# Performance work log

Measured on AMD Instinct MI355X. Metric: run time of the kernel, lower is better.

## Reference

```python
import jax, jax.numpy as jnp
import numpy as np

B, T, D, E = 4, 1024, 1024, 8
HD = 4 * D  # hdim = 4*dim


def setup_inputs() -> dict:
    key = jax.random.key(0)
    k1, k2, k3, k4 = jax.random.split(key, 4)
    std = 0.5 * D ** (-0.5)
    bound = (3.0 ** 0.5) * std
    x = jax.random.normal(k1, (B, T, D), dtype=jnp.float32)
    # router zero-init in source; use small random weights so routing is non-degenerate
    router_w = jax.random.normal(k2, (E, D), dtype=jnp.float32) * 0.02
    expert_fc = jax.random.uniform(k3, (E, D, HD), dtype=jnp.float32, minval=-bound, maxval=bound)
    # proj zero-init in source; use small random so output/backward are non-trivial
    expert_proj = jax.random.normal(k4, (E, D, HD), dtype=jnp.float32) * 0.02
    return {"x": x, "router_w": router_w, "expert_fc": expert_fc, "expert_proj": expert_proj}


def reference(x, router_w, expert_fc, expert_proj):
    # router: Linear(dim, E, bias=False) -> logits [B,T,E]
    logits = jnp.einsum('btd,ed->bte', x, router_w)
    probs = jax.nn.softmax(logits, axis=-1)
    expert_ids = jnp.argmax(probs, axis=-1)  # [B,T]; top-1 (max) routing
    # NOTE: source computes expert_weights (max prob) but does NOT use it in combine.
    mask = jax.nn.one_hot(expert_ids, E, dtype=x.dtype)  # [B,T,E]
    # Dense all-experts compute (faithful to source): h = x @ fc (F.linear with fc.T)
    h = jnp.einsum('btd,edh->ebth', x, expert_fc)
    h = jnp.square(jax.nn.relu(h))  # relu(h)**2
    # expert_output = h @ proj.T (F.linear with proj [dim, hdim])
    out_e = jnp.einsum('ebth,edh->ebtd', h, expert_proj)
    # masked combine: sum_e out_e * (ids == e)
    output = jnp.einsum('ebtd,bte->btd', out_e, mask)
    return output
```

## Files before the change

kernel.cpp:

```cpp
#include <hip/hip_runtime.h>
#include <hip/hip_bf16.h>
#include <stdint.h>

#define NE 8
#define DIM 1024
#define HDIM 4096
#define NTOK 4096
#define KSPLIT 4
#define MAXT 24
#define NT 16

typedef unsigned short ushort_t;
typedef __attribute__((ext_vector_type(4))) float f32x4;
typedef __attribute__((ext_vector_type(8))) short bf16x8;
typedef __attribute__((ext_vector_type(8))) ushort_t u16x8;

#define WAITV(n) asm volatile("s_waitcnt vmcnt(" #n ")" ::: "memory")
#define WAITL0() asm volatile("s_waitcnt lgkmcnt(0)" ::: "memory")
#define WAITL8() asm volatile("s_waitcnt lgkmcnt(8)" ::: "memory")
#define SCHEDB() __builtin_amdgcn_sched_barrier(0)
#define BARRIER() __builtin_amdgcn_s_barrier()

__device__ __forceinline__ ushort_t f2b(float f) {
  union { float f; unsigned u; } c; c.f = f;
  unsigned u = c.u;
  return (ushort_t)((u + 0x7fffu + ((u >> 16) & 1u)) >> 16);
}

__device__ __forceinline__ void gl2lds16(const void* g, void* l) {
  __builtin_amdgcn_global_load_lds(
      (__attribute__((address_space(1))) void*)g,
      (__attribute__((address_space(3))) void*)l, 16, 0, 0);
}

#define PH_MFMA(mh, nh)                                                     \
  { __builtin_amdgcn_s_setprio(1);                                          \
    _Pragma("unroll")                                                       \
    for (int i2 = 0; i2 < 4; ++i2) {                                        \
      _Pragma("unroll")                                                     \
      for (int j2 = 0; j2 < 2; ++j2) {                                      \
        _Pragma("unroll")                                                   \
        for (int kk = 0; kk < 2; ++kk)                                      \
          acc[(mh)*4 + i2][(nh)*2 + j2] =                                   \
            __builtin_amdgcn_mfma_f32_16x16x32_bf16(                        \
              af[i2][kk], bf[(nh)*2 + j2][kk],                              \
              acc[(mh)*4 + i2][(nh)*2 + j2], 0, 0, 0);                      \
      }                                                                     \
    }                                                                       \
    __builtin_amdgcn_s_setprio(0); }

#define LOAD_AF(mh)                                                         \
  { _Pragma("unroll")                                                       \
    for (int i2 = 0; i2 < 4; ++i2) {                                        \
      _Pragma("unroll")                                                     \
      for (int kk = 0; kk < 2; ++kk)                                        \
        af[i2][kk] = *(const bf16x8*)&pA[aBase + ((mh)*64 + i2*16)*64 + ck[kk]]; \
    } }
#define LOAD_BF(nh)                                                         \
  { _Pragma("unroll")                                                       \
    for (int j2 = 0; j2 < 2; ++j2) {                                        \
      _Pragma("unroll")                                                     \
      for (int kk = 0; kk < 2; ++kk)                                        \
        bf[(nh)*2 + j2][kk] = *(const bf16x8*)&pB[bBase + (((nh)*2 + j2)*16)*64 + ck[kk]]; \
    } }

__global__ __launch_bounds__(256) void router_kernel(
    const float* __restrict__ x, const float* __restrict__ rw,
    int* __restrict__ eid, int* __restrict__ rank, int* __restrict__ cnt) {
  __shared__ float w[NE * 1028];
  for (int i = threadIdx.x; i < NE * DIM; i += 256) {
    int e = i >> 10, d = i & 1023;
    w[e * 1028 + d] = rw[i];
  }
  __syncthreads();
  int grp = threadIdx.x >> 3;
  int e = threadIdx.x & 7;
  int t = blockIdx.x * 32 + grp;
  const float4* xr = (const float4*)(x + (size_t)t * DIM);
  const float4* wr = (const float4*)(w + e * 1028);
  float acc = 0.f;
#pragma unroll 4
  for (int i = 0; i < DIM / 4; ++i) {
    float4 xv = xr[i], wv = wr[i];
    acc += xv.x * wv.x + xv.y * wv.y + xv.z * wv.z + xv.w * wv.w;
  }
  float v = acc; int ie = e;
#pragma unroll
  for (int m = 4; m; m >>= 1) {
    float ov = __shfl_xor(v, m, 8);
    int oi = __shfl_xor(ie, m, 8);
    if (ov > v || (ov == v && oi < ie)) { v = ov; ie = oi; }
  }
  if (e == 0) {
    eid[t] = ie;
    rank[t] = atomicAdd(&cnt[ie], 1);
  }
}

__global__ void scan_kernel(const int* __restrict__ cnt, int* __restrict__ offs,
                            int* __restrict__ tile_e, int* __restrict__ tile_m,
                            int* __restrict__ ntiles) {
  if (threadIdx.x == 0) {
    int s = 0, nt = 0;
    for (int e = 0; e < NE; ++e) {
      offs[e] = s;
      int c = cnt[e];
      for (int m = 0; m < c; m += 256) { tile_e[nt] = e; tile_m[nt] = m; ++nt; }
      s += c;
    }
    offs[NE] = s;
    *ntiles = nt;
  }
}

__global__ __launch_bounds__(256) void gather_kernel(
    const float* __restrict__ x, const int* __restrict__ eid,
    const int* __restrict__ rank, const int* __restrict__ offs,
    int* __restrict__ sorted, ushort_t* __restrict__ Xg) {
  int t = blockIdx.x;
  int e = eid[t];
  int pos = offs[e] + rank[t];
  if (threadIdx.x == 0) sorted[pos] = t;
  int i = threadIdx.x;
  float4 v = ((const float4*)(x + (size_t)t * DIM))[i];
  ushort4 o = make_ushort4(f2b(v.x), f2b(v.y), f2b(v.z), f2b(v.w));
  *(ushort4*)(Xg + (size_t)pos * DIM + i * 4) = o;
}

__global__ __launch_bounds__(256) void transpose_fc_kernel(
    const float* __restrict__ fc, ushort_t* __restrict__ fct) {
  __shared__ float tile[64][68];
  int e = blockIdx.z;
  int h0 = blockIdx.x * 64, d0 = blockIdx.y * 64;
  int tid = threadIdx.x;
  int rr = tid >> 4;
  int cc = (tid & 15) * 4;
  const float* src = fc + ((size_t)e * DIM + d0 + rr) * HDIM + h0 + cc;
#pragma unroll
  for (int i = 0; i < 4; ++i) {
    float4 v = *(const float4*)(src + (size_t)(i * 16) * HDIM);
    *(float4*)&tile[rr + i * 16][cc] = v;
  }
  __syncthreads();
  int hr = tid >> 2;
  int dseg = (tid & 3) * 16;
  union { ushort_t s[16]; u16x8 v[2]; } o;
#pragma unroll
  for (int j = 0; j < 16; ++j) o.s[j] = f2b(tile[dseg + j][hr]);
  ushort_t* dst = fct + ((size_t)e * HDIM + h0 + hr) * DIM + d0 + dseg;
  *(u16x8*)dst = o.v[0];
  *(u16x8*)(dst + 8) = o.v[1];
}

#define GEMM_MAIN_LOOP()                                                    \
  stB(0, 0, 0); stB(0, 0, 1); stA(0, 0, 0); stA(0, 0, 1);                   \
  stB(1, 1, 0); stB(1, 1, 1); stA(1, 1, 0);                                 \
  WAITV(6);                                                                 \
  BARRIER();                                                                \
  _Pragma("unroll 1")                                                       \
  for (int T = 0; T < NT; T += 2) {                                         \
    { const ushort_t* pA = As[0]; const ushort_t* pB = Bs[0];               \
                                                                   \
      LOAD_AF(0); LOAD_BF(0);                                               \
      stA(1, T + 1, 1);                                                     \
      WAITL8(); SCHEDB();                                                   \
      BARRIER(); WAITL0(); SCHEDB();                                        \
      PH_MFMA(0, 0);                                                        \
      BARRIER();                                                            \
                                                                   \
      LOAD_BF(1);                                                           \
      BARRIER(); WAITL0(); SCHEDB();                                        \
      PH_MFMA(0, 1);                                                        \
      BARRIER();                                                            \
                                                                   \
      LOAD_AF(1);                                                           \
      if (T + 2 < NT) stB(0, T + 2, 0);                                     \
      BARRIER(); WAITL0(); SCHEDB();                                        \
      PH_MFMA(1, 0);                                                        \
      BARRIER();                                                            \
                                                                   \
      if (T + 2 < NT) { stB(0, T + 2, 1); stA(0, T + 2, 0); WAITV(6); }     \
      else            { WAITV(0); }                                         \
      BARRIER(); SCHEDB();                                                  \
      PH_MFMA(1, 1);                                                        \
      BARRIER();                                                            \
    }                                                                       \
    { const ushort_t* pA = As[1]; const ushort_t* pB = Bs[1];               \
                                                                   \
      LOAD_AF(0); LOAD_BF(0);                                               \
      if (T + 2 < NT) stA(0, T + 2, 1);                                     \
      WAITL8(); SCHEDB();                                                   \
      BARRIER(); WAITL0(); SCHEDB();                                        \
      PH_MFMA(0, 0);                                                        \
      BARRIER();                                                            \
                                                                   \
      LOAD_BF(1);                                                           \
      BARRIER(); WAITL0(); SCHEDB();                                        \
      PH_MFMA(0, 1);                                                        \
      BARRIER();                                                            \
                                                                   \
      LOAD_AF(1);                                                           \
      if (T + 3 < NT) stB(1, T + 3, 0);                                     \
      BARRIER(); WAITL0(); SCHEDB();                                        \
      PH_MFMA(1, 0);                                                        \
      BARRIER();                                                            \
                                                                   \
      if (T + 3 < NT) { stB(1, T + 3, 1); stA(1, T + 3, 0); WAITV(6); }     \
      BARRIER(); SCHEDB();                                                  \
      PH_MFMA(1, 1);                                                        \
      BARRIER();                                                            \
    }                                                                       \
  }

__global__ __launch_bounds__(512, 2) void gemm1_kernel(
    const ushort_t* __restrict__ Xg, const ushort_t* __restrict__ fct,
    const int* __restrict__ offs, const int* __restrict__ tile_e,
    const int* __restrict__ tile_m, const int* __restrict__ ntiles,
    ushort_t* __restrict__ H) {
  __shared__ ushort_t As[2][16384];
  __shared__ ushort_t Bs[2][16384];

  int lin = blockIdx.x + 16 * blockIdx.y;
  int sw = (lin & 7) * 48 + (lin >> 3);
  int bx = sw & 15, by = sw >> 4;
  if (by >= *ntiles) return;

  int e = tile_e[by];
  int mb = tile_m[by];
  int m0 = offs[e];
  int Me = offs[e + 1] - m0;
  int n0 = bx * 256;

  int tid = threadIdx.x;
  int wave = tid >> 6;
  int lane = tid & 63;
  int fr = lane & 15, kq = lane >> 4;
  int wr = wave & 1, wc = wave >> 1;

  int swk = ((tid & 7) ^ ((tid >> 3) & 7)) * 8;
  const ushort_t* aSrc[4]; const ushort_t* bSrc[4];
#pragma unroll
  for (int c = 0; c < 4; ++c) {
    int r = c * 64 + (tid >> 3);
    int rg = mb + r; if (rg >= Me) rg = Me - 1;
    aSrc[c] = Xg + (size_t)(m0 + rg) * DIM + swk;
    bSrc[c] = fct + ((size_t)e * HDIM + n0 + r) * DIM + swk;
  }
  int sdst = wave * 512;

  int aBase = (wr * 128 + fr) * 64;
  int bBase = (wc * 64 + fr) * 64;
  int ck[2] = { (kq ^ (fr & 7)) * 8, ((4 + kq) ^ (fr & 7)) * 8 };

  f32x4 acc[8][4] = {};
  bf16x8 af[4][2], bf[4][2];

  auto stA = [&](int p, int X, int h) __attribute__((always_inline)) {
    int ko = X * 64;
    gl2lds16(aSrc[2 * h] + ko,     &As[p][(2 * h) * 4096 + sdst]);
    gl2lds16(aSrc[2 * h + 1] + ko, &As[p][(2 * h + 1) * 4096 + sdst]);
  };
  auto stB = [&](int p, int X, int h) __attribute__((always_inline)) {
    int ko = X * 64;
    gl2lds16(bSrc[2 * h] + ko,     &Bs[p][(2 * h) * 4096 + sdst]);
    gl2lds16(bSrc[2 * h + 1] + ko, &Bs[p][(2 * h + 1) * 4096 + sdst]);
  };

  GEMM_MAIN_LOOP();

  int cq = kq * 4;
#pragma unroll
  for (int i = 0; i < 8; ++i) {
#pragma unroll
    for (int r = 0; r < 4; ++r) {
      int rl = wr * 128 + i * 16 + cq + r;
      int rg = mb + rl;
      if (rg < Me) {
        ushort_t* dst = H + (size_t)(m0 + rg) * HDIM + n0 + wc * 64 + fr;
#pragma unroll
        for (int j = 0; j < 4; ++j) {
          float v = acc[i][j][r];
          v = fmaxf(v, 0.f);
          dst[j * 16] = f2b(v * v);
        }
      }
    }
  }
}

__global__ __launch_bounds__(512, 2) void gemm2_kernel(
    const ushort_t* __restrict__ Hm, const float* __restrict__ pj,
    const int* __restrict__ offs, const int* __restrict__ tile_e,
    const int* __restrict__ tile_m, const int* __restrict__ ntiles,
    const int* __restrict__ sorted, float* __restrict__ out) {
  __shared__ ushort_t As[2][16384];
  __shared__ ushort_t Bs[2][16384];

  int lin = blockIdx.x + 4 * (blockIdx.y + MAXT * blockIdx.z);
  int sw = (lin & 7) * 48 + (lin >> 3);
  int bx = sw & 3;
  int t2 = sw >> 2;
  int by = t2 % MAXT, bz = t2 / MAXT;
  if (by >= *ntiles) return;

  int e = tile_e[by];
  int mb = tile_m[by];
  int ks = bz;
  int m0 = offs[e];
  int Me = offs[e + 1] - m0;
  int n0 = bx * 256;
  int kbeg = ks * (HDIM / KSPLIT);

  int tid = threadIdx.x;
  int wave = tid >> 6;
  int lane = tid & 63;
  int fr = lane & 15, kq = lane >> 4;
  int wr = wave & 1, wc = wave >> 1;

  int swk = ((tid & 7) ^ ((tid >> 3) & 7)) * 8;
  const ushort_t* aSrc[4];
#pragma unroll
  for (int c = 0; c < 4; ++c) {
    int r = c * 64 + (tid >> 3);
    int rg = mb + r; if (rg >= Me) rg = Me - 1;
    aSrc[c] = Hm + (size_t)(m0 + rg) * HDIM + kbeg + swk;
  }
  int sdst = wave * 512;

  int brow = tid >> 1;
  int bc0 = (tid & 1) * 4;
  const float* bSrcBase = pj + ((size_t)e * DIM + n0 + brow) * HDIM + kbeg + bc0 * 8;
  int bOff[4];
#pragma unroll
  for (int j2 = 0; j2 < 4; ++j2)
    bOff[j2] = brow * 64 + ((bc0 + j2) ^ (brow & 7)) * 8;

  int aBase = (wr * 128 + fr) * 64;
  int bBase = (wc * 64 + fr) * 64;
  int ck[2] = { (kq ^ (fr & 7)) * 8, ((4 + kq) ^ (fr & 7)) * 8 };

  f32x4 acc[8][4] = {};
  bf16x8 af[4][2], bf[4][2];
  float4 bv[8];

  auto loadB = [&](int X) __attribute__((always_inline)) {
    const float* s = bSrcBase + X * 64;
#pragma unroll
    for (int j = 0; j < 8; ++j) bv[j] = *(const float4*)(s + j * 4);
  };
  auto writeB = [&](int pb) __attribute__((always_inline)) {
#pragma unroll
    for (int j2 = 0; j2 < 4; ++j2) {
      union { unsigned u[4]; bf16x8 v; } w;
      float4 a = bv[2 * j2], b = bv[2 * j2 + 1];
      w.u[0] = (unsigned)f2b(a.x) | ((unsigned)f2b(a.y) << 16);
      w.u[1] = (unsigned)f2b(a.z) | ((unsigned)f2b(a.w) << 16);
      w.u[2] = (unsigned)f2b(b.x) | ((unsigned)f2b(b.y) << 16);
      w.u[3] = (unsigned)f2b(b.z) | ((unsigned)f2b(b.w) << 16);
      *(bf16x8*)&Bs[pb][bOff[j2]] = w.v;
    }
  };
  auto stA4 = [&](int p, int X) __attribute__((always_inline)) {
    int ko = X * 64;
#pragma unroll
    for (int c = 0; c < 4; ++c)
      gl2lds16(aSrc[c] + ko, &As[p][c * 4096 + sdst]);
  };

  loadB(0);
  stA4(0, 0);
  WAITV(4);
  writeB(0);
  loadB(1);
  stA4(1, 1);
  WAITV(12);
  WAITL0();
  BARRIER();

#pragma unroll 1
  for (int T = 0; T < NT; T += 2) {
    const bool more = (T + 2 < NT);
    { const ushort_t* pA = As[0]; const ushort_t* pB = Bs[0];
      WAITV(4);
      writeB(1);
      if (more) loadB(T + 2);
      LOAD_AF(0); LOAD_BF(0);
      BARRIER(); WAITL0(); SCHEDB();
      PH_MFMA(0, 0);
      BARRIER();
      LOAD_BF(1);
      BARRIER(); WAITL0(); SCHEDB();
      PH_MFMA(0, 1);
      BARRIER();
      LOAD_AF(1);
      BARRIER(); WAITL0(); SCHEDB();
      PH_MFMA(1, 0);
      BARRIER();
      if (more) { stA4(0, T + 2); WAITV(8); }
      else      { WAITV(0); }
      BARRIER(); SCHEDB();
      PH_MFMA(1, 1);
      BARRIER();
    }
    { const ushort_t* pA = As[1]; const ushort_t* pB = Bs[1];
      if (more) { WAITV(4); writeB(0); loadB(T + 3); }
      LOAD_AF(0); LOAD_BF(0);
      BARRIER(); WAITL0(); SCHEDB();
      PH_MFMA(0, 0);
      BARRIER();
      LOAD_BF(1);
      BARRIER(); WAITL0(); SCHEDB();
      PH_MFMA(0, 1);
      BARRIER();
      LOAD_AF(1);
      BARRIER(); WAITL0(); SCHEDB();
      PH_MFMA(1, 0);
      BARRIER();
      if (more) { stA4(1, T + 3); WAITV(8); }
      BARRIER(); SCHEDB();
      PH_MFMA(1, 1);
      BARRIER();
    }
  }

  int cq = kq * 4;
#pragma unroll
  for (int i = 0; i < 8; ++i) {
#pragma unroll
    for (int r = 0; r < 4; ++r) {
      int rl = wr * 128 + i * 16 + cq + r;
      int rg = mb + rl;
      if (rg < Me) {
        int tok = sorted[m0 + rg];
        float* dst = out + (size_t)tok * DIM + n0 + wc * 64 + fr;
#pragma unroll
        for (int j = 0; j < 4; ++j) atomicAdd(&dst[j * 16], acc[i][j][r]);
      }
    }
  }
}

extern "C" void kernel_launch(void* const* d_in, const int* in_sizes, int n_in,
                              void* d_out, int out_size, void* d_ws, size_t ws_size,
                              hipStream_t stream) {
  const float* x  = (const float*)d_in[0];
  const float* rw = (const float*)d_in[1];
  const float* fc = (const float*)d_in[2];
  const float* pj = (const float*)d_in[3];
  float* out = (float*)d_out;
  char* ws = (char*)d_ws;

  int* eid        = (int*)(ws + 0x0000);
  int* rank       = (int*)(ws + 0x4000);
  int* cnt        = (int*)(ws + 0x8000);
  int* offs       = (int*)(ws + 0x8100);
  int* tile_e     = (int*)(ws + 0x8200);
  int* tile_m     = (int*)(ws + 0x8600);
  int* ntiles     = (int*)(ws + 0x8a00);
  int* sorted     = (int*)(ws + 0x9000);
  ushort_t* Xg    = (ushort_t*)(ws + 0x10000);
  ushort_t* H     = (ushort_t*)(ws + 0x810000);
  ushort_t* W     = (ushort_t*)(ws + 0x2810000);

  hipMemsetAsync(cnt, 0, 32, stream);
  hipMemsetAsync(out, 0, (size_t)NTOK * DIM * sizeof(float), stream);
  router_kernel<<<NTOK / 32, 256, 0, stream>>>(x, rw, eid, rank, cnt);
  scan_kernel<<<1, 64, 0, stream>>>(cnt, offs, tile_e, tile_m, ntiles);
  gather_kernel<<<NTOK, 256, 0, stream>>>(x, eid, rank, offs, sorted, Xg);
  transpose_fc_kernel<<<dim3(HDIM / 64, DIM / 64, NE), 256, 0, stream>>>(fc, W);
  gemm1_kernel<<<dim3(HDIM / 256, MAXT), 512, 0, stream>>>(Xg, W, offs, tile_e, tile_m, ntiles, H);
  gemm2_kernel<<<dim3(DIM / 256, MAXT, KSPLIT), 512, 0, stream>>>(
      H, pj, offs, tile_e, tile_m, ntiles, sorted, out);
}
```

Baseline: 575.3 us.

## Replace atomic split-K combine with partial buffers and a reduce kernel; drop scan kernel

```diff
diff --git a/kernel.cpp b/kernel.cpp
--- a/kernel.cpp
+++ b/kernel.cpp
@@ -31,6 +31,19 @@
   __builtin_amdgcn_global_load_lds(
       (__attribute__((address_space(1))) void*)g,
       (__attribute__((address_space(3))) void*)l, 16, 0, 0);
+}
+
+__device__ __forceinline__ bool tile_lookup(const int* __restrict__ cnt, int by,
+                                            int& e, int& mb, int& m0, int& Me) {
+  int s = 0, acc = 0;
+#pragma unroll
+  for (int ee = 0; ee < NE; ++ee) {
+    int c = cnt[ee];
+    int te = (c + 255) >> 8;
+    if (by >= acc && by < acc + te) { e = ee; mb = (by - acc) << 8; m0 = s; Me = c; }
+    acc += te; s += c;
+  }
+  return by < acc;
 }
 
 #define PH_MFMA(mh, nh)                                                     \
@@ -97,29 +110,16 @@
   }
 }
 
-__global__ void scan_kernel(const int* __restrict__ cnt, int* __restrict__ offs,
-                            int* __restrict__ tile_e, int* __restrict__ tile_m,
-                            int* __restrict__ ntiles) {
-  if (threadIdx.x == 0) {
-    int s = 0, nt = 0;
-    for (int e = 0; e < NE; ++e) {
-      offs[e] = s;
-      int c = cnt[e];
-      for (int m = 0; m < c; m += 256) { tile_e[nt] = e; tile_m[nt] = m; ++nt; }
-      s += c;
-    }
-    offs[NE] = s;
-    *ntiles = nt;
-  }
-}
-
 __global__ __launch_bounds__(256) void gather_kernel(
     const float* __restrict__ x, const int* __restrict__ eid,
-    const int* __restrict__ rank, const int* __restrict__ offs,
+    const int* __restrict__ rank, const int* __restrict__ cnt,
     int* __restrict__ sorted, ushort_t* __restrict__ Xg) {
   int t = blockIdx.x;
   int e = eid[t];
-  int pos = offs[e] + rank[t];
+  int s = 0, off = 0;
+#pragma unroll
+  for (int ee = 0; ee < NE; ++ee) { if (ee == e) off = s; s += cnt[ee]; }
+  int pos = off + rank[t];
   if (threadIdx.x == 0) sorted[pos] = t;
   int i = threadIdx.x;
   float4 v = ((const float4*)(x + (size_t)t * DIM))[i];
@@ -214,21 +214,16 @@
 
 __global__ __launch_bounds__(512, 2) void gemm1_kernel(
     const ushort_t* __restrict__ Xg, const ushort_t* __restrict__ fct,
-    const int* __restrict__ offs, const int* __restrict__ tile_e,
-    const int* __restrict__ tile_m, const int* __restrict__ ntiles,
-    ushort_t* __restrict__ H) {
+    const int* __restrict__ cnt, ushort_t* __restrict__ H) {
   __shared__ ushort_t As[2][16384];
   __shared__ ushort_t Bs[2][16384];
 
   int lin = blockIdx.x + 16 * blockIdx.y;
   int sw = (lin & 7) * 48 + (lin >> 3);
   int bx = sw & 15, by = sw >> 4;
-  if (by >= *ntiles) return;
-
-  int e = tile_e[by];
-  int mb = tile_m[by];
-  int m0 = offs[e];
-  int Me = offs[e + 1] - m0;
+
+  int e, mb, m0, Me;
+  if (!tile_lookup(cnt, by, e, mb, m0, Me)) return;
   int n0 = bx * 256;
 
   int tid = threadIdx.x;
@@ -290,9 +285,7 @@
 
 __global__ __launch_bounds__(512, 2) void gemm2_kernel(
     const ushort_t* __restrict__ Hm, const float* __restrict__ pj,
-    const int* __restrict__ offs, const int* __restrict__ tile_e,
-    const int* __restrict__ tile_m, const int* __restrict__ ntiles,
-    const int* __restrict__ sorted, float* __restrict__ out) {
+    const int* __restrict__ cnt, float* __restrict__ P) {
   __shared__ ushort_t As[2][16384];
   __shared__ ushort_t Bs[2][16384];
 
@@ -301,13 +294,10 @@
   int bx = sw & 3;
   int t2 = sw >> 2;
   int by = t2 % MAXT, bz = t2 / MAXT;
-  if (by >= *ntiles) return;
-
-  int e = tile_e[by];
-  int mb = tile_m[by];
+
+  int e, mb, m0, Me;
+  if (!tile_lookup(cnt, by, e, mb, m0, Me)) return;
   int ks = bz;
-  int m0 = offs[e];
-  int Me = offs[e + 1] - m0;
   int n0 = bx * 256;
   int kbeg = ks * (HDIM / KSPLIT);
 
@@ -396,7 +386,7 @@
       BARRIER(); WAITL0(); SCHEDB();
       PH_MFMA(1, 0);
       BARRIER();
-      if (more) { stA4(0, T + 2); WAITV(8); }
+      if (more) { stA4(0, T + 2); WAITV(12); }
       else      { WAITV(0); }
       BARRIER(); SCHEDB();
       PH_MFMA(1, 1);
@@ -416,7 +406,7 @@
       BARRIER(); WAITL0(); SCHEDB();
       PH_MFMA(1, 0);
       BARRIER();
-      if (more) { stA4(1, T + 3); WAITV(8); }
+      if (more) { stA4(1, T + 3); WAITV(12); }
       BARRIER(); SCHEDB();
       PH_MFMA(1, 1);
       BARRIER();
@@ -431,13 +421,25 @@
       int rl = wr * 128 + i * 16 + cq + r;
       int rg = mb + rl;
       if (rg < Me) {
-        int tok = sorted[m0 + rg];
-        float* dst = out + (size_t)tok * DIM + n0 + wc * 64 + fr;
-#pragma unroll
-        for (int j = 0; j < 4; ++j) atomicAdd(&dst[j * 16], acc[i][j][r]);
+        float* dst = P + ((size_t)ks * NTOK + (m0 + rg)) * DIM + n0 + wc * 64 + fr;
+#pragma unroll
+        for (int j = 0; j < 4; ++j) dst[j * 16] = acc[i][j][r];
       }
     }
   }
+}
+
+__global__ __launch_bounds__(256) void reduce_kernel(
+    const float* __restrict__ P, const int* __restrict__ sorted,
+    float* __restrict__ out) {
+  int pos = blockIdx.x;
+  int tok = sorted[pos];
+  int i = threadIdx.x;
+  size_t base = (size_t)pos * DIM + i * 4;
+  const size_t S = (size_t)NTOK * DIM;
+  f32x4 s = *(const f32x4*)(P + base) + *(const f32x4*)(P + S + base) +
+            *(const f32x4*)(P + 2 * S + base) + *(const f32x4*)(P + 3 * S + base);
+  *(f32x4*)(out + (size_t)tok * DIM + i * 4) = s;
 }
 
 extern "C" void kernel_launch(void* const* d_in, const int* in_sizes, int n_in,
@@ -453,22 +455,17 @@
   int* eid        = (int*)(ws + 0x0000);
   int* rank       = (int*)(ws + 0x4000);
   int* cnt        = (int*)(ws + 0x8000);
-  int* offs       = (int*)(ws + 0x8100);
-  int* tile_e     = (int*)(ws + 0x8200);
-  int* tile_m     = (int*)(ws + 0x8600);
-  int* ntiles     = (int*)(ws + 0x8a00);
   int* sorted     = (int*)(ws + 0x9000);
   ushort_t* Xg    = (ushort_t*)(ws + 0x10000);
   ushort_t* H     = (ushort_t*)(ws + 0x810000);
   ushort_t* W     = (ushort_t*)(ws + 0x2810000);
+  float* P        = (float*)W;
 
   hipMemsetAsync(cnt, 0, 32, stream);
-  hipMemsetAsync(out, 0, (size_t)NTOK * DIM * sizeof(float), stream);
   router_kernel<<<NTOK / 32, 256, 0, stream>>>(x, rw, eid, rank, cnt);
-  scan_kernel<<<1, 64, 0, stream>>>(cnt, offs, tile_e, tile_m, ntiles);
-  gather_kernel<<<NTOK, 256, 0, stream>>>(x, eid, rank, offs, sorted, Xg);
+  gather_kernel<<<NTOK, 256, 0, stream>>>(x, eid, rank, cnt, sorted, Xg);
   transpose_fc_kernel<<<dim3(HDIM / 64, DIM / 64, NE), 256, 0, stream>>>(fc, W);
-  gemm1_kernel<<<dim3(HDIM / 256, MAXT), 512, 0, stream>>>(Xg, W, offs, tile_e, tile_m, ntiles, H);
-  gemm2_kernel<<<dim3(DIM / 256, MAXT, KSPLIT), 512, 0, stream>>>(
-      H, pj, offs, tile_e, tile_m, ntiles, sorted, out);
-}
+  gemm1_kernel<<<dim3(HDIM / 256, MAXT), 512, 0, stream>>>(Xg, W, cnt, H);
+  gemm2_kernel<<<dim3(DIM / 256, MAXT, KSPLIT), 512, 0, stream>>>(H, pj, cnt, P);
+  reduce_kernel<<<NTOK, 256, 0, stream>>>(P, sorted, out);
+}
```

Result: faster. 540.8 us (-6.0%).
